# Kernel tuning notes

Hardware: AMD Instinct MI355X
Metric: run time of the kernel (lower is better)

Reference implementation:

```python
import jax, jax.numpy as jnp
import numpy as np

N, GS, M = 128, 4, 64
C_IN, D, L = 128, 512, 8
LIN_D, OUT_DIM = 128, 1


def _gml_layer(G, h, W, b):
    # h: [N,M,C], W: [GS,P,C], b: [GS,P], G: [N,GS,M,M]
    multi = jnp.einsum('nmc,gpc->gnmp', h, W) + b[:, None, None, :]  # [GS,N,M,P]
    xo = jnp.einsum('ngij,gnjp->ngip', G, multi)                      # [N,GS,M,P]
    xo = jax.nn.relu(xo)
    return jnp.max(xo, axis=1)                                        # goodmax over GS


def setup_inputs() -> dict:
    key = jax.random.key(0)
    ks = jax.random.split(key, 12)
    s = 0.05
    return {
        'G': jax.random.uniform(ks[0], (N, GS, M, M), dtype=jnp.float32),
        'x': jax.random.normal(ks[1], (N, M, C_IN), dtype=jnp.float32),
        'W0': jax.random.normal(ks[2], (GS, D, C_IN), dtype=jnp.float32) * s,
        'b0': jax.random.normal(ks[3], (GS, D), dtype=jnp.float32) * s,
        'W': jax.random.normal(ks[4], (L - 1, GS, D, D), dtype=jnp.float32) * s,
        'b': jax.random.normal(ks[5], (L - 1, GS, D), dtype=jnp.float32) * s,
        'lin1_w': jax.random.normal(ks[6], (LIN_D, D), dtype=jnp.float32) * s,
        'lin1_b': jax.random.normal(ks[7], (LIN_D,), dtype=jnp.float32) * s,
        'lin2_w': jax.random.normal(ks[8], (OUT_DIM, LIN_D), dtype=jnp.float32) * s,
        'lin2_b': jax.random.normal(ks[9], (OUT_DIM,), dtype=jnp.float32) * s,
    }


def reference(G, x, W0, b0, W, b, lin1_w, lin1_b, lin2_w, lin2_b):
    # layer 0: C_IN -> D, shapes differ so no residual
    h = _gml_layer(G, x, W0, b0)  # [N,M,D]

    def step(h, wb):
        w, bb = wb
        return _gml_layer(G, h, w, bb) + h, None  # resnet residual (same shape)

    h, _ = jax.lax.scan(step, h, (W, b))  # L-1 layers of D -> D

    x1 = jnp.einsum('nmd,ed->nme', h, lin1_w) + lin1_b
    x2 = jnp.einsum('nme,oe->nmo', jax.nn.relu(x1), lin2_w) + lin2_b
    return x2  # [N, M, OUT_DIM]
```

## Files before the change

kernel.cpp:

```cpp
#include <hip/hip_runtime.h>

typedef float f32x4 __attribute__((ext_vector_type(4)));
typedef short s16x8 __attribute__((ext_vector_type(8)));
typedef short s16x4 __attribute__((ext_vector_type(4)));
typedef int   i32x4 __attribute__((ext_vector_type(4)));

using abfrag = s16x8;

#define DI __device__ __forceinline__

DI unsigned short f2bf(float x) {
  unsigned u = __builtin_bit_cast(unsigned, x);
  u += 0x7fffu + ((u >> 16) & 1u);
  return (unsigned short)(u >> 16);
}
DI float bf2f(unsigned short h) {
  return __builtin_bit_cast(float, ((unsigned)h) << 16);
}

DI f32x4 MFMA(abfrag a, abfrag b, f32x4 c) {
  return __builtin_amdgcn_mfma_f32_16x16x32_bf16(a, b, c, 0, 0, 0);
}

DI void gld16(void* lds_base, const void* gsrc) {
  __builtin_amdgcn_global_load_lds(
      (const __attribute__((address_space(1))) unsigned int*)gsrc,
      (__attribute__((address_space(3))) unsigned int*)lds_base, 16, 0, 0);
}

#define MEMFENCE asm volatile("" ::: "memory")

__global__ void f2bf_multi(const float* __restrict__ s0, int n0,
                           const float* __restrict__ s1, int n1,
                           const float* __restrict__ s2, int n2,
                           const float* __restrict__ s3, int n3,
                           unsigned short* __restrict__ dst) {
  const int total = n0 + n1 + n2 + n3;
  int i = blockIdx.x * blockDim.x + threadIdx.x;
  const int stride = gridDim.x * blockDim.x;
  for (; i < total; i += stride) {
    const float* s; int off;
    if (i < n0) { s = s0; off = i; }
    else if (i < n0 + n1) { s = s1; off = i - n0; }
    else if (i < n0 + n1 + n2) { s = s2; off = i - n0 - n1; }
    else { s = s3; off = i - n0 - n1 - n2; }
    f32x4 v = ((const f32x4*)s)[off];
    s16x4 o;
#pragma unroll
    for (int j = 0; j < 4; ++j) o[j] = (short)f2bf(v[j]);
    ((s16x4*)dst)[i] = o;
  }
}

template <int C, bool RES>
__global__ __launch_bounds__(256, 2) void gml_layer_kernel(
    const unsigned short* __restrict__ hin,
    const unsigned short* __restrict__ Wb,
    const float* __restrict__ bias,
    const unsigned short* __restrict__ Gb,
    unsigned short* __restrict__ hout) {
  constexpr int NT = C / 64;
  __shared__ short lh[2][64][64];
  __shared__ short lw[2][4][64][64];

  const int tid  = threadIdx.x;
  const int w    = tid >> 6;
  const int lane = tid & 63;
  const int l15  = lane & 15;
  const int l7   = l15 & 7;
  const int gq   = (lane >> 4) & 3;
  const int nl   = w >> 1;
  const int wv   = w & 1;
  const int nn   = blockIdx.x & 63;
  const int pc0  = (blockIdx.x >> 6) * 64;
  const int n    = 2 * nn + nl;
  const int lrow = lane >> 3;
  const int s8   = lane & 7;
  const int lsoff = ((s8 ^ lrow) << 3);

  const unsigned short* hsrc = hin + (size_t)n * 64 * C;

  auto stageH = [&](int kt) {
#pragma unroll
    for (int j = 0; j < 4; ++j)
      gld16(&lh[nl][32 * wv + 8 * j][0],
            hsrc + (size_t)(32 * wv + 8 * j + lrow) * C + kt * 64 + lsoff);
  };
  auto stageW = [&](int buf, int kt) {
#pragma unroll
    for (int j = 0; j < 8; ++j)
      gld16(&lw[buf][w][8 * j][0],
            Wb + (size_t)(w * 512 + pc0 + 8 * j + lrow) * C + kt * 64 + lsoff);
  };
  auto stageG = [&](int nl_) {
#pragma unroll
    for (int j = 0; j < 8; ++j)
      gld16(&lw[nl_][w][8 * j][0],
            Gb + (size_t)((2 * nn + nl_) * 4 + w) * 4096 + (8 * j + lrow) * 64 + lsoff);
  };

  f32x4 acc[4][4][2];
#pragma unroll
  for (int g = 0; g < 4; ++g)
#pragma unroll
    for (int t = 0; t < 4; ++t)
#pragma unroll
      for (int u = 0; u < 2; ++u) acc[g][t][u] = f32x4{0.f, 0.f, 0.f, 0.f};

  stageW(0, 0);
  stageH(0);
  stageW(1, 1);
  asm volatile("s_waitcnt vmcnt(8)" ::: "memory");
  MEMFENCE; __builtin_amdgcn_s_barrier(); MEMFENCE;

  for (int kt = 0; kt < NT; ++kt) {
    const int cur = kt & 1;
#pragma unroll
    for (int ks = 0; ks < 2; ++ks) {
      const int so = ((4 * ks + gq) ^ l7) << 3;
      abfrag a[4];
#pragma unroll
      for (int t = 0; t < 4; ++t)
        a[t] = *(const abfrag*)&lh[nl][16 * t + l15][so];
#pragma unroll
      for (int g = 0; g < 4; ++g)
#pragma unroll
        for (int u = 0; u < 2; ++u) {
          const abfrag b = *(const abfrag*)&lw[cur][g][32 * wv + 16 * u + l15][so];
#pragma unroll
          for (int t = 0; t < 4; ++t) acc[g][t][u] = MFMA(a[t], b, acc[g][t][u]);
        }
    }
    MEMFENCE; __builtin_amdgcn_s_barrier(); MEMFENCE;

    if (kt + 1 < NT) stageH(kt + 1);
    if (kt + 2 < NT) stageW(cur, kt + 2);
    if (kt == NT - 2) stageG(0);
    if (kt == NT - 1) stageG(1);

    if (kt + 1 < NT) {
      asm volatile("s_waitcnt vmcnt(8)" ::: "memory");
    } else {
      asm volatile("s_waitcnt vmcnt(0)" ::: "memory");
    }
    MEMFENCE; __builtin_amdgcn_s_barrier(); MEMFENCE;
  }

  float bv[4][2];
#pragma unroll
  for (int g = 0; g < 4; ++g)
#pragma unroll
    for (int u = 0; u < 2; ++u)
      bv[g][u] = bias[g * 512 + pc0 + 32 * wv + 16 * u + l15];

  f32x4 xmax[4][2];
#pragma unroll
  for (int t = 0; t < 4; ++t)
#pragma unroll
    for (int u = 0; u < 2; ++u) xmax[t][u] = f32x4{0.f, 0.f, 0.f, 0.f};

#pragma unroll
  for (int g = 0; g < 4; ++g) {
    abfrag bb[2][2];
#pragma unroll
    for (int s = 0; s < 2; ++s)
#pragma unroll
      for (int u = 0; u < 2; ++u) {
        abfrag t8;
#pragma unroll
        for (int r = 0; r < 4; ++r) {
          t8[r]     = (short)f2bf(acc[g][s][u][r] + bv[g][u]);
          t8[4 + r] = (short)f2bf(acc[g][s + 2][u][r] + bv[g][u]);
        }
        bb[s][u] = t8;
      }
    f32x4 xg[4][2];
#pragma unroll
    for (int t = 0; t < 4; ++t)
#pragma unroll
      for (int u = 0; u < 2; ++u) xg[t][u] = f32x4{0.f, 0.f, 0.f, 0.f};
#pragma unroll
    for (int t = 0; t < 4; ++t) {
      const short* grow = &lw[nl][g][16 * t + l15][0];
#pragma unroll
      for (int s = 0; s < 2; ++s) {
        const int slot = 2 * s + (gq >> 1);
        const int e1 = ((slot ^ l7) << 3) + ((gq & 1) << 2);
        const int e2 = (((slot + 4) ^ l7) << 3) + ((gq & 1) << 2);
        s16x4 alo = *(const s16x4*)(grow + e1);
        s16x4 ahi = *(const s16x4*)(grow + e2);
        abfrag a;
#pragma unroll
        for (int j = 0; j < 4; ++j) { a[j] = alo[j]; a[4 + j] = ahi[j]; }
#pragma unroll
        for (int u = 0; u < 2; ++u) xg[t][u] = MFMA(a, bb[s][u], xg[t][u]);
      }
    }
#pragma unroll
    for (int t = 0; t < 4; ++t)
#pragma unroll
      for (int u = 0; u < 2; ++u)
#pragma unroll
        for (int r = 0; r < 4; ++r)
          xmax[t][u][r] = fmaxf(xmax[t][u][r], xg[t][u][r]);
  }

#pragma unroll
  for (int t = 0; t < 4; ++t)
#pragma unroll
    for (int u = 0; u < 2; ++u)
#pragma unroll
      for (int r = 0; r < 4; ++r) {
        const int m = 16 * t + 4 * gq + r;
        const int d = pc0 + 32 * wv + 16 * u + l15;
        float v = xmax[t][u][r];
        if constexpr (RES) v += bf2f(hin[(size_t)(n * 64 + m) * C + d]);
        hout[(size_t)(n * 64 + m) * 512 + d] = f2bf(v);
      }
}

__global__ __launch_bounds__(256, 2) void final_kernel(
    const unsigned short* __restrict__ hin,
    const float* __restrict__ w1,
    const float* __restrict__ b1,
    const float* __restrict__ w2,
    const float* __restrict__ b2,
    float* __restrict__ out) {
  constexpr int KT = 64, LW = 72, C = 512, NT = C / KT;
  __shared__ short sh_h[2][64][LW];
  __shared__ short sh_w[2][128][LW];
  __shared__ float red[4][64];
  const int tid = threadIdx.x;
  const int wv  = tid >> 6;
  const int l15 = tid & 15;
  const int gq  = (tid >> 4) & 3;
  const int n   = blockIdx.x;
  const int srow = tid >> 3;
  const int scol = (tid & 7) * 8;
  const unsigned short* hsrc = hin + (size_t)n * 64 * C;

  f32x4 acc[4][2];
#pragma unroll
  for (int t = 0; t < 4; ++t)
#pragma unroll
    for (int u = 0; u < 2; ++u) acc[t][u] = f32x4{0.f, 0.f, 0.f, 0.f};

  i32x4 hr[2], wr[4];
#pragma unroll
  for (int p = 0; p < 2; ++p)
    hr[p] = *(const i32x4*)(hsrc + (srow + p * 32) * C + scol);
#pragma unroll
  for (int p = 0; p < 4; ++p) {
    const float* s = w1 + (srow + p * 32) * C + scol;
    f32x4 v0 = *(const f32x4*)s;
    f32x4 v1 = *(const f32x4*)(s + 4);
    s16x8 o;
#pragma unroll
    for (int j = 0; j < 4; ++j) { o[j] = (short)f2bf(v0[j]); o[4 + j] = (short)f2bf(v1[j]); }
    wr[p] = __builtin_bit_cast(i32x4, o);
  }
#pragma unroll
  for (int p = 0; p < 2; ++p) *(i32x4*)&sh_h[0][srow + p * 32][scol] = hr[p];
#pragma unroll
  for (int p = 0; p < 4; ++p) *(i32x4*)&sh_w[0][srow + p * 32][scol] = wr[p];

  for (int kt = 0; kt < NT; ++kt) {
    const int cur = kt & 1;
    if (kt + 1 < NT) {
#pragma unroll
      for (int p = 0; p < 2; ++p)
        hr[p] = *(const i32x4*)(hsrc + (srow + p * 32) * C + (kt + 1) * KT + scol);
#pragma unroll
      for (int p = 0; p < 4; ++p) {
        const float* s = w1 + (srow + p * 32) * C + (kt + 1) * KT + scol;
        f32x4 v0 = *(const f32x4*)s;
        f32x4 v1 = *(const f32x4*)(s + 4);
        s16x8 o;
#pragma unroll
        for (int j = 0; j < 4; ++j) { o[j] = (short)f2bf(v0[j]); o[4 + j] = (short)f2bf(v1[j]); }
        wr[p] = __builtin_bit_cast(i32x4, o);
      }
    }
    __syncthreads();
#pragma unroll
    for (int ks = 0; ks < 2; ++ks) {
      abfrag a[4], b[2];
#pragma unroll
      for (int t = 0; t < 4; ++t)
        a[t] = *(const abfrag*)&sh_h[cur][16 * t + l15][ks * 32 + gq * 8];
#pragma unroll
      for (int u = 0; u < 2; ++u)
        b[u] = *(const abfrag*)&sh_w[cur][32 * wv + 16 * u + l15][ks * 32 + gq * 8];
#pragma unroll
      for (int t = 0; t < 4; ++t)
#pragma unroll
        for (int u = 0; u < 2; ++u) acc[t][u] = MFMA(a[t], b[u], acc[t][u]);
    }
    if (kt + 1 < NT) {
#pragma unroll
      for (int p = 0; p < 2; ++p) *(i32x4*)&sh_h[1 - cur][srow + p * 32][scol] = hr[p];
#pragma unroll
      for (int p = 0; p < 4; ++p) *(i32x4*)&sh_w[1 - cur][srow + p * 32][scol] = wr[p];
    }
  }

  float b1v[2], w2v[2];
#pragma unroll
  for (int u = 0; u < 2; ++u) {
    b1v[u] = b1[32 * wv + 16 * u + l15];
    w2v[u] = w2[32 * wv + 16 * u + l15];
  }
  float part[4][4];
#pragma unroll
  for (int t = 0; t < 4; ++t)
#pragma unroll
    for (int r = 0; r < 4; ++r) {
      float s0 = 0.f;
#pragma unroll
      for (int u = 0; u < 2; ++u)
        s0 += fmaxf(acc[t][u][r] + b1v[u], 0.f) * w2v[u];
      part[t][r] = s0;
    }
#pragma unroll
  for (int t = 0; t < 4; ++t)
#pragma unroll
    for (int r = 0; r < 4; ++r)
#pragma unroll
      for (int msk = 1; msk < 16; msk <<= 1)
        part[t][r] += __shfl_xor(part[t][r], msk);
  if (l15 == 0) {
#pragma unroll
    for (int t = 0; t < 4; ++t)
#pragma unroll
      for (int r = 0; r < 4; ++r) red[wv][16 * t + 4 * gq + r] = part[t][r];
  }
  __syncthreads();
  if (tid < 64)
    out[(size_t)n * 64 + tid] =
        red[0][tid] + red[1][tid] + red[2][tid] + red[3][tid] + b2[0];
}

extern "C" void kernel_launch(void* const* d_in, const int* in_sizes, int n_in,
                              void* d_out, int out_size, void* d_ws, size_t ws_size,
                              hipStream_t stream) {
  const float* G   = (const float*)d_in[0];
  const float* x   = (const float*)d_in[1];
  const float* W0  = (const float*)d_in[2];
  const float* b0  = (const float*)d_in[3];
  const float* W   = (const float*)d_in[4];
  const float* b   = (const float*)d_in[5];
  const float* l1w = (const float*)d_in[6];
  const float* l1b = (const float*)d_in[7];
  const float* l2w = (const float*)d_in[8];
  const float* l2b = (const float*)d_in[9];
  float* out = (float*)d_out;

  char* p = (char*)d_ws;
  unsigned short* W0b = (unsigned short*)p; p += (size_t)4 * 512 * 128 * 2;
  unsigned short* Wb  = (unsigned short*)p; p += (size_t)7 * 4 * 512 * 512 * 2;
  unsigned short* Gb  = (unsigned short*)p; p += (size_t)128 * 4 * 64 * 64 * 2;
  unsigned short* xb  = (unsigned short*)p; p += (size_t)128 * 64 * 128 * 2;
  unsigned short* hA  = (unsigned short*)p; p += (size_t)128 * 64 * 512 * 2;
  unsigned short* hB  = (unsigned short*)p; p += (size_t)128 * 64 * 512 * 2;

  const int n0 = 4 * 512 * 128 / 4;
  const int n1 = 7 * 4 * 512 * 512 / 4;
  const int n2 = 128 * 4 * 64 * 64 / 4;
  const int n3 = 128 * 64 * 128 / 4;
  f2bf_multi<<<2048, 256, 0, stream>>>(W0, n0, W, n1, G, n2, x, n3, W0b);

  gml_layer_kernel<128, false><<<512, 256, 0, stream>>>(xb, W0b, b0, Gb, hA);
  const unsigned short* src = hA;
  unsigned short* dst = hB;
  for (int i = 0; i < 7; ++i) {
    gml_layer_kernel<512, true><<<512, 256, 0, stream>>>(
        src, Wb + (size_t)i * 4 * 512 * 512, b + (size_t)i * 4 * 512, Gb, dst);
    const unsigned short* t = src; src = dst; dst = (unsigned short*)t;
  }
  final_kernel<<<128, 256, 0, stream>>>(src, l1w, l1b, l2w, l2b, out);
}
```

Baseline: 215.1 us.

## Use 512-thread blocks with K=32 tiles and read G directly from global

The GML layer kernel moves from 256 to 512 threads per block. Each wave now owns a 16-column slice instead of 32, which halves the accumulator registers, and the K tile shrinks from 64 to 32 so that H and W share one double-buffered stage. G is no longer staged through LDS; the second GEMM reads its fragments straight from global memory. The aim is higher occupancy and less LDS, at the cost of twice as many barriers per K and uncoalesced 8-byte global reads of G in the epilogue.

```diff
diff --git a/kernel.cpp b/kernel.cpp
--- a/kernel.cpp
+++ b/kernel.cpp
@@ -53,170 +53,133 @@
 }
 
 template <int C, bool RES>
-__global__ __launch_bounds__(256, 2) void gml_layer_kernel(
+__global__ __launch_bounds__(512, 4) void gml_layer_kernel(
     const unsigned short* __restrict__ hin,
     const unsigned short* __restrict__ Wb,
     const float* __restrict__ bias,
     const unsigned short* __restrict__ Gb,
     unsigned short* __restrict__ hout) {
-  constexpr int NT = C / 64;
-  __shared__ short lh[2][64][64];
-  __shared__ short lw[2][4][64][64];
+  constexpr int NT = C / 32;
+  __shared__ short lh[2][2][64][32];
+  __shared__ short lw[2][4][64][32];
 
   const int tid  = threadIdx.x;
   const int w    = tid >> 6;
   const int lane = tid & 63;
   const int l15  = lane & 15;
-  const int l7   = l15 & 7;
   const int gq   = (lane >> 4) & 3;
-  const int nl   = w >> 1;
-  const int wv   = w & 1;
+  const int nl   = w >> 2;
+  const int cv   = w & 3;
   const int nn   = blockIdx.x & 63;
   const int pc0  = (blockIdx.x >> 6) * 64;
   const int n    = 2 * nn + nl;
-  const int lrow = lane >> 3;
-  const int s8   = lane & 7;
-  const int lsoff = ((s8 ^ lrow) << 3);
+  const int drow  = lane >> 2;
+  const int soff  = (((lane & 3) ^ (drow & 3)) << 3);
+  const int so = ((gq ^ (l15 & 3)) << 3);
 
   const unsigned short* hsrc = hin + (size_t)n * 64 * C;
 
-  auto stageH = [&](int kt) {
-#pragma unroll
-    for (int j = 0; j < 4; ++j)
-      gld16(&lh[nl][32 * wv + 8 * j][0],
-            hsrc + (size_t)(32 * wv + 8 * j + lrow) * C + kt * 64 + lsoff);
+  const int hn   = w >> 2;
+  const int hr0  = 16 * (w & 3);
+  const int wg   = w & 3;
+  const int wr0  = 32 * (w >> 2);
+  const unsigned short* hstage = hin + ((size_t)(2 * nn + hn) * 64 + hr0 + drow) * C + soff;
+
+  auto stage = [&](int buf, int kt) {
+    gld16(&lh[buf][hn][hr0][0], hstage + kt * 32);
+#pragma unroll
+    for (int j = 0; j < 2; ++j)
+      gld16(&lw[buf][wg][wr0 + 16 * j][0],
+            Wb + (size_t)(wg * 512 + pc0 + wr0 + 16 * j + drow) * C + kt * 32 + soff);
   };
-  auto stageW = [&](int buf, int kt) {
-#pragma unroll
-    for (int j = 0; j < 8; ++j)
-      gld16(&lw[buf][w][8 * j][0],
-            Wb + (size_t)(w * 512 + pc0 + 8 * j + lrow) * C + kt * 64 + lsoff);
-  };
-  auto stageG = [&](int nl_) {
-#pragma unroll
-    for (int j = 0; j < 8; ++j)
-      gld16(&lw[nl_][w][8 * j][0],
-            Gb + (size_t)((2 * nn + nl_) * 4 + w) * 4096 + (8 * j + lrow) * 64 + lsoff);
-  };
-
-  f32x4 acc[4][4][2];
+
+  f32x4 acc[4][4];
 #pragma unroll
   for (int g = 0; g < 4; ++g)
 #pragma unroll
-    for (int t = 0; t < 4; ++t)
-#pragma unroll
-      for (int u = 0; u < 2; ++u) acc[g][t][u] = f32x4{0.f, 0.f, 0.f, 0.f};
-
-  stageW(0, 0);
-  stageH(0);
-  stageW(1, 1);
-  asm volatile("s_waitcnt vmcnt(8)" ::: "memory");
+    for (int t = 0; t < 4; ++t) acc[g][t] = f32x4{0.f, 0.f, 0.f, 0.f};
+
+  stage(0, 0);
+  stage(1, 1);
+  asm volatile("s_waitcnt vmcnt(3)" ::: "memory");
   MEMFENCE; __builtin_amdgcn_s_barrier(); MEMFENCE;
 
   for (int kt = 0; kt < NT; ++kt) {
     const int cur = kt & 1;
-#pragma unroll
-    for (int ks = 0; ks < 2; ++ks) {
-      const int so = ((4 * ks + gq) ^ l7) << 3;
-      abfrag a[4];
-#pragma unroll
-      for (int t = 0; t < 4; ++t)
-        a[t] = *(const abfrag*)&lh[nl][16 * t + l15][so];
-#pragma unroll
-      for (int g = 0; g < 4; ++g)
-#pragma unroll
-        for (int u = 0; u < 2; ++u) {
-          const abfrag b = *(const abfrag*)&lw[cur][g][32 * wv + 16 * u + l15][so];
-#pragma unroll
-          for (int t = 0; t < 4; ++t) acc[g][t][u] = MFMA(a[t], b, acc[g][t][u]);
-        }
-    }
+    abfrag a[4];
+#pragma unroll
+    for (int t = 0; t < 4; ++t)
+      a[t] = *(const abfrag*)&lh[cur][nl][16 * t + l15][so];
+#pragma unroll
+    for (int g = 0; g < 4; ++g) {
+      const abfrag b = *(const abfrag*)&lw[cur][g][16 * cv + l15][so];
+#pragma unroll
+      for (int t = 0; t < 4; ++t) acc[g][t] = MFMA(a[t], b, acc[g][t]);
+    }
+    if (kt == NT - 1) break;
     MEMFENCE; __builtin_amdgcn_s_barrier(); MEMFENCE;
 
-    if (kt + 1 < NT) stageH(kt + 1);
-    if (kt + 2 < NT) stageW(cur, kt + 2);
-    if (kt == NT - 2) stageG(0);
-    if (kt == NT - 1) stageG(1);
-
-    if (kt + 1 < NT) {
-      asm volatile("s_waitcnt vmcnt(8)" ::: "memory");
+    if (kt + 2 < NT) {
+      stage(cur, kt + 2);
+      asm volatile("s_waitcnt vmcnt(3)" ::: "memory");
     } else {
       asm volatile("s_waitcnt vmcnt(0)" ::: "memory");
     }
     MEMFENCE; __builtin_amdgcn_s_barrier(); MEMFENCE;
   }
 
-  float bv[4][2];
-#pragma unroll
-  for (int g = 0; g < 4; ++g)
-#pragma unroll
-    for (int u = 0; u < 2; ++u)
-      bv[g][u] = bias[g * 512 + pc0 + 32 * wv + 16 * u + l15];
-
-  f32x4 xmax[4][2];
+  float bv[4];
+#pragma unroll
+  for (int g = 0; g < 4; ++g) bv[g] = bias[g * 512 + pc0 + 16 * cv + l15];
+
+  f32x4 xmax[4];
+#pragma unroll
+  for (int t = 0; t < 4; ++t) xmax[t] = f32x4{0.f, 0.f, 0.f, 0.f};
+
+  const unsigned short* gbase = Gb + (size_t)n * 4 * 4096;
+#pragma unroll
+  for (int g = 0; g < 4; ++g) {
+    abfrag bb[2];
+#pragma unroll
+    for (int s = 0; s < 2; ++s) {
+      abfrag t8;
+#pragma unroll
+      for (int r = 0; r < 4; ++r) {
+        t8[r]     = (short)f2bf(acc[g][s][r] + bv[g]);
+        t8[4 + r] = (short)f2bf(acc[g][s + 2][r] + bv[g]);
+      }
+      bb[s] = t8;
+    }
+    const unsigned short* gg = gbase + g * 4096;
+#pragma unroll
+    for (int t = 0; t < 4; ++t) {
+      f32x4 xg = f32x4{0.f, 0.f, 0.f, 0.f};
+#pragma unroll
+      for (int s = 0; s < 2; ++s) {
+        const unsigned short* gp = gg + (16 * t + l15) * 64 + 16 * s + 4 * gq;
+        s16x4 alo = *(const s16x4*)gp;
+        s16x4 ahi = *(const s16x4*)(gp + 32);
+        abfrag a;
+#pragma unroll
+        for (int j = 0; j < 4; ++j) { a[j] = alo[j]; a[4 + j] = ahi[j]; }
+        xg = MFMA(a, bb[s], xg);
+      }
+#pragma unroll
+      for (int r = 0; r < 4; ++r)
+        xmax[t][r] = fmaxf(xmax[t][r], xg[r]);
+    }
+  }
+
+  const int d = pc0 + 16 * cv + l15;
 #pragma unroll
   for (int t = 0; t < 4; ++t)
 #pragma unroll
-    for (int u = 0; u < 2; ++u) xmax[t][u] = f32x4{0.f, 0.f, 0.f, 0.f};
-
-#pragma unroll
-  for (int g = 0; g < 4; ++g) {
-    abfrag bb[2][2];
-#pragma unroll
-    for (int s = 0; s < 2; ++s)
-#pragma unroll
-      for (int u = 0; u < 2; ++u) {
-        abfrag t8;
-#pragma unroll
-        for (int r = 0; r < 4; ++r) {
-          t8[r]     = (short)f2bf(acc[g][s][u][r] + bv[g][u]);
-          t8[4 + r] = (short)f2bf(acc[g][s + 2][u][r] + bv[g][u]);
-        }
-        bb[s][u] = t8;
-      }
-    f32x4 xg[4][2];
-#pragma unroll
-    for (int t = 0; t < 4; ++t)
-#pragma unroll
-      for (int u = 0; u < 2; ++u) xg[t][u] = f32x4{0.f, 0.f, 0.f, 0.f};
-#pragma unroll
-    for (int t = 0; t < 4; ++t) {
-      const short* grow = &lw[nl][g][16 * t + l15][0];
-#pragma unroll
-      for (int s = 0; s < 2; ++s) {
-        const int slot = 2 * s + (gq >> 1);
-        const int e1 = ((slot ^ l7) << 3) + ((gq & 1) << 2);
-        const int e2 = (((slot + 4) ^ l7) << 3) + ((gq & 1) << 2);
-        s16x4 alo = *(const s16x4*)(grow + e1);
-        s16x4 ahi = *(const s16x4*)(grow + e2);
-        abfrag a;
-#pragma unroll
-        for (int j = 0; j < 4; ++j) { a[j] = alo[j]; a[4 + j] = ahi[j]; }
-#pragma unroll
-        for (int u = 0; u < 2; ++u) xg[t][u] = MFMA(a, bb[s][u], xg[t][u]);
-      }
-    }
-#pragma unroll
-    for (int t = 0; t < 4; ++t)
-#pragma unroll
-      for (int u = 0; u < 2; ++u)
-#pragma unroll
-        for (int r = 0; r < 4; ++r)
-          xmax[t][u][r] = fmaxf(xmax[t][u][r], xg[t][u][r]);
-  }
-
-#pragma unroll
-  for (int t = 0; t < 4; ++t)
-#pragma unroll
-    for (int u = 0; u < 2; ++u)
-#pragma unroll
-      for (int r = 0; r < 4; ++r) {
-        const int m = 16 * t + 4 * gq + r;
-        const int d = pc0 + 32 * wv + 16 * u + l15;
-        float v = xmax[t][u][r];
-        if constexpr (RES) v += bf2f(hin[(size_t)(n * 64 + m) * C + d]);
-        hout[(size_t)(n * 64 + m) * 512 + d] = f2bf(v);
-      }
+    for (int r = 0; r < 4; ++r) {
+      const int m = 16 * t + 4 * gq + r;
+      float v = xmax[t][r];
+      if constexpr (RES) v += bf2f(hin[(size_t)(n * 64 + m) * C + d]);
+      hout[(size_t)(n * 64 + m) * 512 + d] = f2bf(v);
+    }
 }
 
 __global__ __launch_bounds__(256, 2) void final_kernel(
@@ -369,11 +332,11 @@
   const int n3 = 128 * 64 * 128 / 4;
   f2bf_multi<<<2048, 256, 0, stream>>>(W0, n0, W, n1, G, n2, x, n3, W0b);
 
-  gml_layer_kernel<128, false><<<512, 256, 0, stream>>>(xb, W0b, b0, Gb, hA);
+  gml_layer_kernel<128, false><<<512, 512, 0, stream>>>(xb, W0b, b0, Gb, hA);
   const unsigned short* src = hA;
   unsigned short* dst = hB;
   for (int i = 0; i < 7; ++i) {
-    gml_layer_kernel<512, true><<<512, 256, 0, stream>>>(
+    gml_layer_kernel<512, true><<<512, 512, 0, stream>>>(
         src, Wb + (size_t)i * 4 * 512 * 512, b + (size_t)i * 4 * 512, Gb, dst);
     const unsigned short* t = src; src = dst; dst = (unsigned short*)t;
   }
```

After: 371.4 us. 1.73x slower.

## Retile GML layer to one graph per block with 128-wide columns and K=32 steps

Applied to the files above, without the earlier changes.

Each block now handles a single graph n with 128 output columns (4 waves × 32), instead of two graphs with 64 columns each. The K tile shrinks from 64 to 32 and the loop becomes a simple double buffer that prefetches the next tile before computing, with one barrier per iteration. G is staged into the reused weight buffer at the end. This halves redundant W loads per block and simplifies the pipeline, at the cost of more iterations and barriers and smaller per-stage transfers. The conversion kernel's grid is also doubled.

```diff
diff --git a/kernel.cpp b/kernel.cpp
--- a/kernel.cpp
+++ b/kernel.cpp
@@ -59,9 +59,10 @@
     const float* __restrict__ bias,
     const unsigned short* __restrict__ Gb,
     unsigned short* __restrict__ hout) {
-  constexpr int NT = C / 64;
-  __shared__ short lh[2][64][64];
-  __shared__ short lw[2][4][64][64];
+  constexpr int NT = C / 32;
+  __shared__ short lh[2][64][32];
+  __shared__ short lw[2][4][128][32];
+  auto lgv = (short(*)[64][64]) & lw[0][0][0][0];
 
   const int tid  = threadIdx.x;
   const int w    = tid >> 6;
@@ -69,35 +70,30 @@
   const int l15  = lane & 15;
   const int l7   = l15 & 7;
   const int gq   = (lane >> 4) & 3;
-  const int nl   = w >> 1;
-  const int wv   = w & 1;
-  const int nn   = blockIdx.x & 63;
-  const int pc0  = (blockIdx.x >> 6) * 64;
-  const int n    = 2 * nn + nl;
-  const int lrow = lane >> 3;
-  const int s8   = lane & 7;
-  const int lsoff = ((s8 ^ lrow) << 3);
+  const int n    = blockIdx.x & 127;
+  const int pc0  = (blockIdx.x >> 7) * 128;
+
+  const int soff32 = (((lane & 3) ^ ((lane >> 3) & 3)) << 3);
+  const int lrow8  = lane >> 3;
+  const int soff64 = (((lane & 7) ^ lrow8) << 3);
+  const int so = ((gq ^ ((l15 >> 1) & 3)) << 3);
 
   const unsigned short* hsrc = hin + (size_t)n * 64 * C;
 
-  auto stageH = [&](int kt) {
-#pragma unroll
-    for (int j = 0; j < 4; ++j)
-      gld16(&lh[nl][32 * wv + 8 * j][0],
-            hsrc + (size_t)(32 * wv + 8 * j + lrow) * C + kt * 64 + lsoff);
+  auto stage = [&](int buf, int kt) {
+    gld16(&lh[buf][16 * w][0],
+          hsrc + (size_t)(16 * w + (lane >> 2)) * C + kt * 32 + soff32);
+#pragma unroll
+    for (int j = 0; j < 8; ++j)
+      gld16(&lw[buf][w][16 * j][0],
+            Wb + (size_t)(w * 512 + pc0 + 16 * j + (lane >> 2)) * C + kt * 32 + soff32);
   };
-  auto stageW = [&](int buf, int kt) {
+  auto stageG = [&]() {
 #pragma unroll
     for (int j = 0; j < 8; ++j)
-      gld16(&lw[buf][w][8 * j][0],
-            Wb + (size_t)(w * 512 + pc0 + 8 * j + lrow) * C + kt * 64 + lsoff);
+      gld16(&lgv[w][8 * j][0],
+            Gb + (size_t)(n * 4 + w) * 4096 + (8 * j + lrow8) * 64 + soff64);
   };
-  auto stageG = [&](int nl_) {
-#pragma unroll
-    for (int j = 0; j < 8; ++j)
-      gld16(&lw[nl_][w][8 * j][0],
-            Gb + (size_t)((2 * nn + nl_) * 4 + w) * 4096 + (8 * j + lrow) * 64 + lsoff);
-  };
 
   f32x4 acc[4][4][2];
 #pragma unroll
@@ -107,43 +103,30 @@
 #pragma unroll
       for (int u = 0; u < 2; ++u) acc[g][t][u] = f32x4{0.f, 0.f, 0.f, 0.f};
 
-  stageW(0, 0);
-  stageH(0);
-  stageW(1, 1);
-  asm volatile("s_waitcnt vmcnt(8)" ::: "memory");
-  MEMFENCE; __builtin_amdgcn_s_barrier(); MEMFENCE;
-
+  stage(0, 0);
+  __syncthreads();
+
+#pragma unroll 2
   for (int kt = 0; kt < NT; ++kt) {
     const int cur = kt & 1;
-#pragma unroll
-    for (int ks = 0; ks < 2; ++ks) {
-      const int so = ((4 * ks + gq) ^ l7) << 3;
-      abfrag a[4];
-#pragma unroll
-      for (int t = 0; t < 4; ++t)
-        a[t] = *(const abfrag*)&lh[nl][16 * t + l15][so];
-#pragma unroll
-      for (int g = 0; g < 4; ++g)
-#pragma unroll
-        for (int u = 0; u < 2; ++u) {
-          const abfrag b = *(const abfrag*)&lw[cur][g][32 * wv + 16 * u + l15][so];
-#pragma unroll
-          for (int t = 0; t < 4; ++t) acc[g][t][u] = MFMA(a[t], b, acc[g][t][u]);
-        }
-    }
-    MEMFENCE; __builtin_amdgcn_s_barrier(); MEMFENCE;
-
-    if (kt + 1 < NT) stageH(kt + 1);
-    if (kt + 2 < NT) stageW(cur, kt + 2);
-    if (kt == NT - 2) stageG(0);
-    if (kt == NT - 1) stageG(1);
-
-    if (kt + 1 < NT) {
-      asm volatile("s_waitcnt vmcnt(8)" ::: "memory");
-    } else {
-      asm volatile("s_waitcnt vmcnt(0)" ::: "memory");
-    }
-    MEMFENCE; __builtin_amdgcn_s_barrier(); MEMFENCE;
+    if (kt + 1 < NT) stage(cur ^ 1, kt + 1);
+    else stageG();
+    MEMFENCE;
+
+    abfrag a[4];
+#pragma unroll
+    for (int t = 0; t < 4; ++t)
+      a[t] = *(const abfrag*)&lh[cur][16 * t + l15][so];
+#pragma unroll
+    for (int g = 0; g < 4; ++g)
+#pragma unroll
+      for (int u = 0; u < 2; ++u) {
+        const abfrag b = *(const abfrag*)&lw[cur][g][32 * w + 16 * u + l15][so];
+#pragma unroll
+        for (int t = 0; t < 4; ++t) acc[g][t][u] = MFMA(a[t], b, acc[g][t][u]);
+      }
+
+    __syncthreads();
   }
 
   float bv[4][2];
@@ -151,7 +134,7 @@
   for (int g = 0; g < 4; ++g)
 #pragma unroll
     for (int u = 0; u < 2; ++u)
-      bv[g][u] = bias[g * 512 + pc0 + 32 * wv + 16 * u + l15];
+      bv[g][u] = bias[g * 512 + pc0 + 32 * w + 16 * u + l15];
 
   f32x4 xmax[4][2];
 #pragma unroll
@@ -181,7 +164,7 @@
       for (int u = 0; u < 2; ++u) xg[t][u] = f32x4{0.f, 0.f, 0.f, 0.f};
 #pragma unroll
     for (int t = 0; t < 4; ++t) {
-      const short* grow = &lw[nl][g][16 * t + l15][0];
+      const short* grow = &lgv[g][16 * t + l15][0];
 #pragma unroll
       for (int s = 0; s < 2; ++s) {
         const int slot = 2 * s + (gq >> 1);
@@ -212,7 +195,7 @@
 #pragma unroll
       for (int r = 0; r < 4; ++r) {
         const int m = 16 * t + 4 * gq + r;
-        const int d = pc0 + 32 * wv + 16 * u + l15;
+        const int d = pc0 + 32 * w + 16 * u + l15;
         float v = xmax[t][u][r];
         if constexpr (RES) v += bf2f(hin[(size_t)(n * 64 + m) * C + d]);
         hout[(size_t)(n * 64 + m) * 512 + d] = f2bf(v);
@@ -367,7 +350,7 @@
   const int n1 = 7 * 4 * 512 * 512 / 4;
   const int n2 = 128 * 4 * 64 * 64 / 4;
   const int n3 = 128 * 64 * 128 / 4;
-  f2bf_multi<<<2048, 256, 0, stream>>>(W0, n0, W, n1, G, n2, x, n3, W0b);
+  f2bf_multi<<<4096, 256, 0, stream>>>(W0, n0, W, n1, G, n2, x, n3, W0b);
 
   gml_layer_kernel<128, false><<<512, 256, 0, stream>>>(xb, W0b, b0, Gb, hA);
   const unsigned short* src = hA;
```

New measurement: 222.4 us. +3.4%, slower.
